# Kernel optimization log

Hardware: AMD Instinct MI355X
Metric: run time of the kernel (lower is better)

Reference implementation:

```python
import jax, jax.numpy as jnp
import numpy as np

BETA = 0.25  # commitment loss weight (standard VQ-VAE)


def setup_inputs() -> dict:
    key = jax.random.key(0)
    ks = jax.random.split(key, 6)
    B, C, H, W = 8, 64, 64, 64
    K = 8192  # codebook size
    return {
        "z": jax.random.normal(ks[0], (B, C, H, W), dtype=jnp.float32),
        "pre_w": jax.random.normal(ks[1], (C, C), dtype=jnp.float32) * (1.0 / np.sqrt(C)),
        "pre_b": jax.random.normal(ks[2], (C,), dtype=jnp.float32) * 0.02,
        "emb": jax.random.normal(ks[3], (K, C), dtype=jnp.float32),
        "post_w": jax.random.normal(ks[4], (C, C), dtype=jnp.float32) * (1.0 / np.sqrt(C)),
        "post_b": jax.random.normal(ks[5], (C,), dtype=jnp.float32) * 0.02,
    }


def reference(z, pre_w, pre_b, emb, post_w, post_b):
    B, C, H, W = z.shape
    # pre_quant_conv: 1x1 conv == channel-mixing matmul
    ze = jnp.einsum("bchw,oc->bohw", z, pre_w) + pre_b[None, :, None, None]
    # flatten to tokens [N, C]
    zf = ze.transpose(0, 2, 3, 1).reshape(-1, C)
    # squared L2 distances to codebook: ||z||^2 - 2 z.e + ||e||^2
    d = (jnp.sum(zf * zf, axis=1, keepdims=True)
         - 2.0 * (zf @ emb.T)
         + jnp.sum(emb * emb, axis=1)[None, :])  # [N, K]
    idx = jnp.argmin(d, axis=1)  # [N]
    q = emb[idx].reshape(B, H, W, C).transpose(0, 3, 1, 2)  # [B,C,H,W]
    # VQ losses
    codebook_loss = jnp.mean((jax.lax.stop_gradient(ze) - q) ** 2)
    commit_loss = BETA * jnp.mean((ze - jax.lax.stop_gradient(q)) ** 2)
    loss = codebook_loss + commit_loss
    # straight-through estimator
    quant = ze + jax.lax.stop_gradient(q - ze)
    # post_quant_conv: 1x1 conv
    out = jnp.einsum("bchw,oc->bohw", quant, post_w) + post_b[None, :, None, None]
    return out, loss
```

## Files before the change

kernel.cpp:

```cpp
#include <hip/hip_runtime.h>
#include <stdint.h>

#define HW 4096
#define NTOK 32768
#define KCB 8192
#define YSPLIT 8
#define KCOV (KCB / YSPLIT)
#define NCHUNK (KCOV / 64)
#define MARGIN 0.0148925781f
#define ACC_BIAS 3145728.0f

typedef __bf16 bf16x8 __attribute__((ext_vector_type(8)));
typedef float f32x16 __attribute__((ext_vector_type(16)));
typedef unsigned int uint;
typedef unsigned short u16;
typedef unsigned long long u64;

static __device__ inline u16 f2bf(float f) {
    uint u = __float_as_uint(f);
    return (u16)((u + 0x7FFFu + ((u >> 16) & 1u)) >> 16);
}
static __device__ inline float bf2f(u16 h) {
    return __uint_as_float(((uint)h) << 16);
}
static __device__ inline uint fsort(float f) {
    uint u = __float_as_uint(f);
    return u ^ ((uint)((int)u >> 31) | 0x80000000u);
}
static __device__ inline uint umin2(uint a, uint b) { return a < b ? a : b; }
static __device__ inline uint umax2(uint a, uint b) { return a > b ? a : b; }
static __device__ inline uint umed3(uint a, uint b, uint c) {
    return umax2(umin2(a, b), umin2(umax2(a, b), c));
}

__global__ __launch_bounds__(256) void prep_kernel(
    const float* __restrict__ z, const float* __restrict__ pre_w,
    const float* __restrict__ pre_b, const float* __restrict__ emb,
    const float* __restrict__ post_w, const float* __restrict__ post_b,
    u16* __restrict__ zq, u16* __restrict__ embq,
    float* __restrict__ ee, float* __restrict__ eebs,
    float* __restrict__ embWb, float* __restrict__ loss_out,
    int* __restrict__ flagcnt)
{
    __shared__ __attribute__((aligned(16))) float wt[64 * 64];
    __shared__ __attribute__((aligned(16))) float zt[64 * 64];
    __shared__ float bls[64];
    const int t  = threadIdx.x;
    const int bx = blockIdx.x;

    if (bx >= 768) {
        const int k0  = (bx - 768) * 64;
        const int tok = t >> 2;
        const int og  = t & 3;

        for (int i = t; i < 64 * 64; i += 256) {
            int o = i >> 6, c = i & 63;
            wt[c * 64 + o] = post_w[i];
        }
        if (t < 64) bls[t] = post_b[t];
        {
            const float4* qr = (const float4*)(emb + (size_t)(k0 + tok) * 64);
            #pragma unroll
            for (int p = 0; p < 4; ++p) {
                const int c0 = og * 16 + p * 4;
                float4 v = qr[c0 >> 2];
                zt[(c0+0) * 64 + tok] = v.x;
                zt[(c0+1) * 64 + tok] = v.y;
                zt[(c0+2) * 64 + tok] = v.z;
                zt[(c0+3) * 64 + tok] = v.w;
            }
        }
        __syncthreads();

        const int w    = t >> 6;
        const int lane = t & 63;
        float acc[16];
        #pragma unroll
        for (int j = 0; j < 16; ++j) acc[j] = 0.f;
        for (int c = 0; c < 64; ++c) {
            const float qv = zt[c * 64 + lane];
            #pragma unroll
            for (int g = 0; g < 4; ++g) {
                float4 w4 = *(const float4*)(wt + c * 64 + w * 16 + g * 4);
                acc[g*4+0] = fmaf(qv, w4.x, acc[g*4+0]);
                acc[g*4+1] = fmaf(qv, w4.y, acc[g*4+1]);
                acc[g*4+2] = fmaf(qv, w4.z, acc[g*4+2]);
                acc[g*4+3] = fmaf(qv, w4.w, acc[g*4+3]);
            }
        }
        __syncthreads();
        #pragma unroll
        for (int j = 0; j < 16; ++j)
            zt[(w * 16 + j) * 64 + lane] = acc[j] + bls[w * 16 + j];
        __syncthreads();
        {
            float4* orow = (float4*)(embWb + (size_t)(k0 + tok) * 64 + og * 16);
            #pragma unroll
            for (int p = 0; p < 4; ++p) {
                const int c0 = og * 16 + p * 4;
                float4 v;
                v.x = zt[(c0+0) * 64 + tok];
                v.y = zt[(c0+1) * 64 + tok];
                v.z = zt[(c0+2) * 64 + tok];
                v.w = zt[(c0+3) * 64 + tok];
                orow[p] = v;
            }
        }
        return;
    }

    if (bx >= 512) {
        const int k   = (bx - 512) * 32 + (t >> 3);
        const int sub = t & 7;
        const float4* er = (const float4*)(emb + (size_t)k * 64 + sub * 8);
        float4 v0 = er[0], v1 = er[1];

        float s = v0.x*v0.x + v0.y*v0.y + v0.z*v0.z + v0.w*v0.w
                + v1.x*v1.x + v1.y*v1.y + v1.z*v1.z + v1.w*v1.w;
        s += __shfl_xor(s, 1, 64);
        s += __shfl_xor(s, 2, 64);
        s += __shfl_xor(s, 4, 64);
        if (sub == 0) {
            ee[k] = s;
            eebs[k] = fmaf(1024.f, s, ACC_BIAS + 262144.f);
        }

        float vals[8] = {-64.f*v0.x, -64.f*v0.y, -64.f*v0.z, -64.f*v0.w,
                         -64.f*v1.x, -64.f*v1.y, -64.f*v1.z, -64.f*v1.w};
        u16 hb[8], lb[8];
        #pragma unroll
        for (int c = 0; c < 8; ++c) {
            hb[c] = f2bf(vals[c]);
            lb[c] = f2bf(vals[c] - bf2f(hb[c]));
        }
        uint4 uh, ul;
        uh.x = (uint)hb[0] | ((uint)hb[1] << 16);
        uh.y = (uint)hb[2] | ((uint)hb[3] << 16);
        uh.z = (uint)hb[4] | ((uint)hb[5] << 16);
        uh.w = (uint)hb[6] | ((uint)hb[7] << 16);
        ul.x = (uint)lb[0] | ((uint)lb[1] << 16);
        ul.y = (uint)lb[2] | ((uint)lb[3] << 16);
        ul.z = (uint)lb[4] | ((uint)lb[5] << 16);
        ul.w = (uint)lb[6] | ((uint)lb[7] << 16);

        const int sw = k & 7;
        uint4* out = (uint4*)(embq + (size_t)k * 128);
        out[sub ^ sw]       = uh;
        out[(8 + sub) ^ sw] = ul;
        if (bx == 512 && t == 0) { loss_out[0] = 0.f; *flagcnt = 0; }
        return;
    }

    const int tok0 = bx * 64;
    const int b    = tok0 >> 12;
    const int hw0  = tok0 & 4095;

    for (int i = t; i < 64 * 64; i += 256) {
        int o = i >> 6, c = i & 63;
        wt[c * 64 + o] = pre_w[i];
    }
    if (t < 64) bls[t] = pre_b[t];
    {
        const int tl = t & 63;
        #pragma unroll
        for (int rr = 0; rr < 16; ++rr) {
            const int c = (t >> 6) + rr * 4;
            zt[c * 64 + tl] = z[(size_t)b * (64 * HW) + (size_t)c * HW + hw0 + tl];
        }
    }
    __syncthreads();

    const int tok = t >> 2;
    const int og  = t & 3;
    const int n   = tok0 + tok;

    float acc[16];
    #pragma unroll
    for (int j = 0; j < 16; ++j) acc[j] = 0.f;

    for (int c = 0; c < 64; ++c) {
        const float zv = zt[c * 64 + tok];
        #pragma unroll
        for (int g = 0; g < 4; ++g) {
            float4 w4 = *(const float4*)(wt + c * 64 + og * 16 + g * 4);
            acc[g*4+0] = fmaf(zv, w4.x, acc[g*4+0]);
            acc[g*4+1] = fmaf(zv, w4.y, acc[g*4+1]);
            acc[g*4+2] = fmaf(zv, w4.z, acc[g*4+2]);
            acc[g*4+3] = fmaf(zv, w4.w, acc[g*4+3]);
        }
    }
    #pragma unroll
    for (int j = 0; j < 16; ++j) acc[j] = 32.f * (acc[j] + bls[og * 16 + j]);

    uint uh[8], ul[8];
    #pragma unroll
    for (int j = 0; j < 8; ++j) {
        float v0 = acc[2*j], v1 = acc[2*j+1];
        u16 h0 = f2bf(v0), h1 = f2bf(v1);
        u16 l0 = f2bf(v0 - bf2f(h0)), l1 = f2bf(v1 - bf2f(h1));
        uh[j] = (uint)h0 | ((uint)h1 << 16);
        ul[j] = (uint)l0 | ((uint)l1 << 16);
    }
    uint4* zh = (uint4*)(zq + (size_t)n * 128 + og * 16);
    uint4* zl = (uint4*)(zq + (size_t)n * 128 + 64 + og * 16);
    zh[0] = *(uint4*)&uh[0]; zh[1] = *(uint4*)&uh[4];
    zl[0] = *(uint4*)&ul[0]; zl[1] = *(uint4*)&ul[4];
}

__global__ __launch_bounds__(256, 4) void dist_kernel(
    const u16* __restrict__ zq, const u16* __restrict__ embq,
    const float* __restrict__ eebs, uint* __restrict__ halfbb,
    uint* __restrict__ halfss)
{
    __shared__ __attribute__((aligned(16))) char smem[32768];
    __shared__ uint gbk[128];

    const int t    = threadIdx.x;
    const int w    = t >> 6;
    const int l    = t & 63;
    const int col  = l & 31;
    const int half = l >> 5;
    const int tok0 = blockIdx.x * 128;
    const int y    = blockIdx.y;
    const int kbase = y * KCOV;

    bf16x8 ah[4], al[4];
    {
        const u16* zrow = zq + (size_t)(tok0 + w * 32 + col) * 128;
        #pragma unroll
        for (int s = 0; s < 4; ++s) {
            ah[s] = *(const bf16x8*)(zrow + s*16 + half*8);
            al[s] = *(const bf16x8*)(zrow + 64 + s*16 + half*8);
        }
    }

    const int sw = col & 7;
    int boh[4][2], bol[4][2];
    #pragma unroll
    for (int s = 0; s < 4; ++s)
        #pragma unroll
        for (int ct = 0; ct < 2; ++ct) {
            const int nl = ct * 32 + col;
            boh[s][ct] = nl * 256 + (((s*2 + half) ^ sw) << 4);
            bol[s][ct] = nl * 256 + (((8 + s*2 + half) ^ sw) << 4);
        }

    uint bb[16], ss[16];
    #pragma unroll
    for (int r = 0; r < 16; ++r) { bb[r] = 0xFFFFFFFFu; ss[r] = 0xFFFFFFFFu; }

    float e0 = eebs[kbase + col];
    float e1 = eebs[kbase + 32 + col];

    {
        const char* g = (const char*)embq + (size_t)kbase * 256;
        #pragma unroll
        for (int i = 0; i < 4; ++i) {
            int off = i * 4096 + t * 16;
            __builtin_amdgcn_global_load_lds(
                (const __attribute__((address_space(1))) void*)(g + off),
                (__attribute__((address_space(3))) void*)(smem + off), 16, 0, 0);
        }
    }

    for (int kt = 0; kt < NCHUNK; ++kt) {
        __syncthreads();
        if (kt + 1 < NCHUNK) {
            const char* g = (const char*)embq + (size_t)kbase * 256 + (size_t)(kt + 1) * 16384;
            char* ld = smem + ((kt + 1) & 1) * 16384;
            #pragma unroll
            for (int i = 0; i < 4; ++i) {
                int off = i * 4096 + t * 16;
                __builtin_amdgcn_global_load_lds(
                    (const __attribute__((address_space(1))) void*)(g + off),
                    (__attribute__((address_space(3))) void*)(ld + off), 16, 0, 0);
            }
        }
        const char* buf = smem + (kt & 1) * 16384;

        float e0n = 0.f, e1n = 0.f;
        if (kt + 1 < NCHUNK) {
            e0n = eebs[kbase + (kt+1)*64 + col];
            e1n = eebs[kbase + (kt+1)*64 + 32 + col];
        }

        f32x16 a0, a1;
        #pragma unroll
        for (int r = 0; r < 16; ++r) { a0[r] = e0; a1[r] = e1; }

        #pragma unroll
        for (int s = 0; s < 4; ++s) {
            bf16x8 bh0 = *(const bf16x8*)(buf + boh[s][0]);
            bf16x8 bh1 = *(const bf16x8*)(buf + boh[s][1]);
            bf16x8 bl0 = *(const bf16x8*)(buf + bol[s][0]);
            bf16x8 bl1 = *(const bf16x8*)(buf + bol[s][1]);
            a0 = __builtin_amdgcn_mfma_f32_32x32x16_bf16(ah[s], bh0, a0, 0, 0, 0);
            a1 = __builtin_amdgcn_mfma_f32_32x32x16_bf16(ah[s], bh1, a1, 0, 0, 0);
            a0 = __builtin_amdgcn_mfma_f32_32x32x16_bf16(ah[s], bl0, a0, 0, 0, 0);
            a1 = __builtin_amdgcn_mfma_f32_32x32x16_bf16(ah[s], bl1, a1, 0, 0, 0);
            a0 = __builtin_amdgcn_mfma_f32_32x32x16_bf16(al[s], bh0, a0, 0, 0, 0);
            a1 = __builtin_amdgcn_mfma_f32_32x32x16_bf16(al[s], bh1, a1, 0, 0, 0);
        }

        const uint i0 = (uint)(kt * 64 + col);
        const uint i1 = i0 + 32;
        #pragma unroll
        for (int r = 0; r < 16; ++r) {
            const uint p0 = (__float_as_uint(a0[r]) << 10) + i0;
            const uint p1 = (__float_as_uint(a1[r]) << 10) + i1;
            ss[r] = umin2(ss[r], umed3(bb[r], p0, p1));
            bb[r] = umin2(umin2(bb[r], p0), p1);
        }
        e0 = e0n; e1 = e1n;
    }

    __syncthreads();
    uint* keyt = (uint*)smem;
    #pragma unroll
    for (int r = 0; r < 16; ++r) {
        const int tl = w*32 + (r & 3) + 8*(r >> 2) + 4*half;
        keyt[tl * 32 + col] = bb[r];
    }
    __syncthreads();
    if (t < 128) {
        uint gb = keyt[t * 32 + (t & 31)];
        #pragma unroll 4
        for (int j = 1; j < 32; ++j)
            gb = umin2(gb, keyt[t * 32 + ((j + t) & 31)]);
        gbk[t] = gb;
    }
    __syncthreads();
    #pragma unroll
    for (int r = 0; r < 16; ++r) {
        const int tl = w*32 + (r & 3) + 8*(r >> 2) + 4*half;
        const uint mykey = bb[r];
        keyt[tl * 32 + col] = (mykey == gbk[tl]) ? ss[r] : mykey;
    }
    __syncthreads();
    if (t < 128) {
        uint sv = keyt[t * 32 + (t & 31)];
        #pragma unroll 4
        for (int j = 1; j < 32; ++j)
            sv = umin2(sv, keyt[t * 32 + ((j + t) & 31)]);
        halfbb[(size_t)y * NTOK + tok0 + t] = gbk[t];
        halfss[(size_t)y * NTOK + tok0 + t] = sv;
    }
}

__global__ __launch_bounds__(256) void merge_kernel(
    const uint* __restrict__ halfbb, const uint* __restrict__ halfss,
    uint* __restrict__ bestidx, u64* __restrict__ bestkeyB,
    int* __restrict__ flagcnt, int* __restrict__ flaglist)
{
    const int n = blockIdx.x * 256 + threadIdx.x;
    uint m1 = 0xFFFFFFFFu, m2 = 0xFFFFFFFFu, smin = 0xFFFFFFFFu;
    int ywin = 0;
    #pragma unroll
    for (int y = 0; y < YSPLIT; ++y) {
        const uint kb = halfbb[(size_t)y * NTOK + n];
        if (kb < m1) { m2 = m1; m1 = kb; ywin = y; }
        else if (kb < m2) m2 = kb;
        smin = umin2(smin, halfss[(size_t)y * NTOK + n]);
    }
    const uint bv_u = m1 >> 12;
    const uint sv_u = umin2(m2, smin) >> 12;
    const float gap = (float)(sv_u - bv_u) * 9.765625e-4f;
    const bool flag = (gap < MARGIN) | (bv_u < (128u << 10));
    bestidx[n]  = flag ? 0xFFFFFFFFu : (uint)(ywin * 1024) + (m1 & 1023u);
    bestkeyB[n] = ~0ull;
    if (flag) {
        int pos = atomicAdd(flagcnt, 1);
        flaglist[pos] = n;
    }
}

__global__ __launch_bounds__(256) void cleanup_kernel(
    const u16* __restrict__ zq, const float* __restrict__ emb,
    const float* __restrict__ ee, const int* __restrict__ flagcnt,
    const int* __restrict__ flaglist, u64* __restrict__ bestkeyB)
{
    __shared__ __attribute__((aligned(16))) float zf[64];
    __shared__ u64 smin;
    const int cnt = *flagcnt;
    const int t = threadIdx.x;

    for (int job = blockIdx.x; job < cnt * 32; job += 2048) {
        const int fi    = job >> 5;
        const int slice = job & 31;
        const int tok   = flaglist[fi];
        if (t == 0) smin = ~0ull;
        if (t < 64) {
            const u16* zr = zq + (size_t)tok * 128;
            zf[t] = (bf2f(zr[t]) + bf2f(zr[64 + t])) * 0.03125f;
        }
        __syncthreads();

        const int k = slice * 256 + t;
        const float4* er = (const float4*)(emb + (size_t)k * 64);
        float d = 0.f;
        #pragma unroll
        for (int jj = 0; jj < 16; ++jj) {
            float4 e = er[jj];
            float4 zv = *(const float4*)&zf[4*jj];
            d = fmaf(e.x, zv.x, fmaf(e.y, zv.y, fmaf(e.z, zv.z, fmaf(e.w, zv.w, d))));
        }
        float dd = fmaf(-2.f, d, ee[k]);
        u64 key = ((u64)fsort(dd) << 32) | (uint)k;
        #pragma unroll
        for (int off = 32; off > 0; off >>= 1) {
            u64 o = __shfl_down(key, off, 64);
            key = (o < key) ? o : key;
        }
        if ((t & 63) == 0) atomicMin(&smin, key);
        __syncthreads();
        if (t == 0) atomicMin(&bestkeyB[tok], smin);
        __syncthreads();
    }
}

__global__ __launch_bounds__(256) void finish_kernel(
    const float* __restrict__ emb, const float* __restrict__ embWb,
    const uint* __restrict__ bestidx, const u64* __restrict__ bestkeyB,
    const u16* __restrict__ zq, float* __restrict__ out,
    float* __restrict__ loss_out)
{
    __shared__ __attribute__((aligned(16))) float ot[64 * 64];
    __shared__ int idxs[64];
    __shared__ float red[4];
    const int t = threadIdx.x;
    const int tok0 = blockIdx.x * 64;
    const int b    = tok0 >> 12;
    const int hw0  = tok0 & 4095;

    if (t < 64) {
        const uint raw = bestidx[tok0 + t];
        idxs[t] = (raw == 0xFFFFFFFFu) ? (int)(bestkeyB[tok0 + t] & 0xFFFFFFFFull)
                                       : (int)raw;
    }
    __syncthreads();

    const int tok = t >> 2;
    const int og  = t & 3;
    const int n   = tok0 + tok;
    const int idx = idxs[tok];

    {
        const float4* orow = (const float4*)(embWb + (size_t)idx * 64 + og * 16);
        #pragma unroll
        for (int p = 0; p < 4; ++p) {
            const int c0 = og * 16 + p * 4;
            float4 v = orow[p];
            ot[(c0+0) * 64 + tok] = v.x;
            ot[(c0+1) * 64 + tok] = v.y;
            ot[(c0+2) * 64 + tok] = v.z;
            ot[(c0+3) * 64 + tok] = v.w;
        }
    }

    float lsum = 0.f;
    {
        const float4* qr = (const float4*)(emb + (size_t)idx * 64 + og * 16);
        const uint4* zh = (const uint4*)(zq + (size_t)n * 128 + og * 16);
        const uint4* zl = (const uint4*)(zq + (size_t)n * 128 + 64 + og * 16);
        #pragma unroll
        for (int h = 0; h < 2; ++h) {
            uint4 uh = zh[h], ul = zl[h];
            float4 q0 = qr[h*2], q1 = qr[h*2+1];
            const uint uhv[4] = {uh.x, uh.y, uh.z, uh.w};
            const uint ulv[4] = {ul.x, ul.y, ul.z, ul.w};
            const float qv[8] = {q0.x, q0.y, q0.z, q0.w, q1.x, q1.y, q1.z, q1.w};
            #pragma unroll
            for (int p = 0; p < 4; ++p) {
                float z0 = (bf2f((u16)(uhv[p] & 0xFFFF)) + bf2f((u16)(ulv[p] & 0xFFFF))) * 0.03125f;
                float z1 = (bf2f((u16)(uhv[p] >> 16))    + bf2f((u16)(ulv[p] >> 16)))    * 0.03125f;
                float d0 = z0 - qv[2*p];
                float d1 = z1 - qv[2*p+1];
                lsum += d0 * d0 + d1 * d1;
            }
        }
    }
    __syncthreads();

    {
        const int w    = t >> 6;
        const int lane = t & 63;
        float* op = out + (size_t)b * (64 * HW) + hw0 + lane;
        #pragma unroll
        for (int j = 0; j < 16; ++j)
            op[(size_t)(w * 16 + j) * HW] = ot[(w * 16 + j) * 64 + lane];
    }

    #pragma unroll
    for (int off = 32; off > 0; off >>= 1) lsum += __shfl_down(lsum, off, 64);
    if ((t & 63) == 0) red[t >> 6] = lsum;
    __syncthreads();
    if (t == 0) {
        const float tot = red[0] + red[1] + red[2] + red[3];
        atomicAdd(loss_out, tot * (1.25f / 2097152.f));
    }
}

extern "C" void kernel_launch(void* const* d_in, const int* in_sizes, int n_in,
                              void* d_out, int out_size, void* d_ws, size_t ws_size,
                              hipStream_t stream)
{
    const float* z      = (const float*)d_in[0];
    const float* pre_w  = (const float*)d_in[1];
    const float* pre_b  = (const float*)d_in[2];
    const float* emb    = (const float*)d_in[3];
    const float* post_w = (const float*)d_in[4];
    const float* post_b = (const float*)d_in[5];
    float* outp = (float*)d_out;
    float* loss_out = outp + (size_t)NTOK * 64;

    u16*   zq       = (u16*)d_ws;
    float* ee       = (float*)(zq + (size_t)NTOK * 128);
    float* eebs     = ee + KCB;
    u16*   embq     = (u16*)(eebs + KCB);
    u64*   bestkeyB = (u64*)(embq + (size_t)KCB * 128);
    uint*  bestidx  = (uint*)(bestkeyB + NTOK);
    int*   flagcnt  = (int*)(bestidx + NTOK);
    int*   flaglist = flagcnt + 1;
    uint*  halfbb   = (uint*)(flaglist + NTOK);
    uint*  halfss   = halfbb + (size_t)YSPLIT * NTOK;
    float* embWb    = (float*)(halfss + (size_t)YSPLIT * NTOK);

    prep_kernel<<<896, 256, 0, stream>>>(z, pre_w, pre_b, emb, post_w, post_b,
                                         zq, embq, ee, eebs, embWb, loss_out, flagcnt);
    dist_kernel<<<dim3(NTOK / 128, YSPLIT), 256, 0, stream>>>(zq, embq, eebs, halfbb, halfss);
    merge_kernel<<<NTOK / 256, 256, 0, stream>>>(halfbb, halfss, bestidx, bestkeyB,
                                                 flagcnt, flaglist);
    cleanup_kernel<<<2048, 256, 0, stream>>>(zq, emb, ee, flagcnt, flaglist, bestkeyB);
    finish_kernel<<<NTOK / 64, 256, 0, stream>>>(emb, embWb, bestidx, bestkeyB, zq,
                                                 outp, loss_out);
}
```

Before: 237.7 us.

## Triple-buffer codebook tiles in LDS and stage codebook norms in shared memory

```diff
diff --git a/kernel.cpp b/kernel.cpp
--- a/kernel.cpp
+++ b/kernel.cpp
@@ -212,8 +212,9 @@
     const float* __restrict__ eebs, uint* __restrict__ halfbb,
     uint* __restrict__ halfss)
 {
-    __shared__ __attribute__((aligned(16))) char smem[32768];
+    __shared__ __attribute__((aligned(16))) char smem[3 * 16384 + 4096];
     __shared__ uint gbk[128];
+    float* eebs_lds = (float*)(smem + 3 * 16384);
 
     const int t    = threadIdx.x;
     const int w    = t >> 6;
@@ -249,25 +250,41 @@
     #pragma unroll
     for (int r = 0; r < 16; ++r) { bb[r] = 0xFFFFFFFFu; ss[r] = 0xFFFFFFFFu; }
 
-    float e0 = eebs[kbase + col];
-    float e1 = eebs[kbase + 32 + col];
-
     {
-        const char* g = (const char*)embq + (size_t)kbase * 256;
+        float4 ev = *(const float4*)(eebs + kbase + t * 4);
+        *(float4*)(eebs_lds + t * 4) = ev;
+    }
+    asm volatile("s_waitcnt lgkmcnt(0)" ::: "memory");
+
+    #pragma unroll
+    for (int c = 0; c < 2; ++c) {
+        const char* g = (const char*)embq + (size_t)kbase * 256 + (size_t)c * 16384;
+        char* ld = smem + c * 16384;
         #pragma unroll
         for (int i = 0; i < 4; ++i) {
             int off = i * 4096 + t * 16;
             __builtin_amdgcn_global_load_lds(
                 (const __attribute__((address_space(1))) void*)(g + off),
-                (__attribute__((address_space(3))) void*)(smem + off), 16, 0, 0);
-        }
-    }
+                (__attribute__((address_space(3))) void*)(ld + off), 16, 0, 0);
+        }
+    }
+
+    float e0 = 0.f, e1 = 0.f;
 
     for (int kt = 0; kt < NCHUNK; ++kt) {
-        __syncthreads();
-        if (kt + 1 < NCHUNK) {
-            const char* g = (const char*)embq + (size_t)kbase * 256 + (size_t)(kt + 1) * 16384;
-            char* ld = smem + ((kt + 1) & 1) * 16384;
+        if (kt < NCHUNK - 1)
+            asm volatile("s_waitcnt vmcnt(4)\n\ts_barrier" ::: "memory");
+        else
+            asm volatile("s_waitcnt vmcnt(0)\n\ts_barrier" ::: "memory");
+
+        if (kt == 0) {
+            e0 = eebs_lds[col];
+            e1 = eebs_lds[32 + col];
+        }
+
+        if (kt + 2 < NCHUNK) {
+            const char* g = (const char*)embq + (size_t)kbase * 256 + (size_t)(kt + 2) * 16384;
+            char* ld = smem + ((kt + 2) % 3) * 16384;
             #pragma unroll
             for (int i = 0; i < 4; ++i) {
                 int off = i * 4096 + t * 16;
@@ -276,13 +293,7 @@
                     (__attribute__((address_space(3))) void*)(ld + off), 16, 0, 0);
             }
         }
-        const char* buf = smem + (kt & 1) * 16384;
-
-        float e0n = 0.f, e1n = 0.f;
-        if (kt + 1 < NCHUNK) {
-            e0n = eebs[kbase + (kt+1)*64 + col];
-            e1n = eebs[kbase + (kt+1)*64 + 32 + col];
-        }
+        const char* buf = smem + (kt % 3) * 16384;
 
         f32x16 a0, a1;
         #pragma unroll
@@ -302,6 +313,12 @@
             a1 = __builtin_amdgcn_mfma_f32_32x32x16_bf16(al[s], bh1, a1, 0, 0, 0);
         }
 
+        if (kt + 1 < NCHUNK) {
+            e0 = eebs_lds[(kt + 1) * 64 + col];
+            e1 = eebs_lds[(kt + 1) * 64 + 32 + col];
+            asm volatile("" :: "v"(e0), "v"(e1));
+        }
+
         const uint i0 = (uint)(kt * 64 + col);
         const uint i1 = i0 + 32;
         #pragma unroll
@@ -311,7 +328,6 @@
             ss[r] = umin2(ss[r], umed3(bb[r], p0, p1));
             bb[r] = umin2(umin2(bb[r], p0), p1);
         }
-        e0 = e0n; e1 = e1n;
     }
 
     __syncthreads();
```

New measurement: 247.9 us. 1.04x slower.
